# Performance work log

Hardware: AMD Instinct MI355X
Metric: run time of the kernel (lower is better)

The kernel has to match this reference:

```python
import jax, jax.numpy as jnp
import numpy as np
from jax import lax

N, C, H, W = 8, 512, 28, 28
G = 8                     # attention groups
QKP = 32                  # qk_planes = out/groups/2
VP = 64                   # v_planes = branch/groups
BP = 512                  # branch_planes
HW = H * W
EPS = 1e-5                # BatchNorm eps (eval mode, running_mean=0, running_var=1)


def bn(x, gamma, beta, axis=1):
    shape = [1] * x.ndim
    shape[axis] = x.shape[axis]
    g = gamma.reshape(shape)
    b = beta.reshape(shape)
    return x * (g / jnp.sqrt(1.0 + EPS)) + b


def conv2d(x, w, groups=1):
    return lax.conv_general_dilated(
        x, w, (1, 1), 'SAME',
        dimension_numbers=('NCHW', 'OIHW', 'NCHW'),
        feature_group_count=groups)


def setup_inputs() -> dict:
    key = jax.random.key(0)
    ks = jax.random.split(key, 16)
    pe_dim = 2 * QKP + VP  # 128
    inp = {
        'x':        jax.random.normal(ks[0], (N, C, H, W), jnp.float32),
        'qkv_w':    jax.random.normal(ks[1], (BP * 2, C), jnp.float32) * np.sqrt(1.0 / C),
        'g_qkv':    jax.random.normal(ks[2], (BP * 2,), jnp.float32) * 0.1 + 1.0,
        'b_qkv':    jax.random.normal(ks[3], (BP * 2,), jnp.float32) * 0.1,
        'g_sim':    jax.random.normal(ks[4], (G * 3,), jnp.float32) * 0.1 + 1.0,
        'b_sim':    jax.random.normal(ks[5], (G * 3,), jnp.float32) * 0.1,
        'g_out':    jax.random.normal(ks[6], (BP * 2,), jnp.float32) * 0.1 + 1.0,
        'b_out':    jax.random.normal(ks[7], (BP * 2,), jnp.float32) * 0.1,
        'relative': jax.random.normal(ks[8], (pe_dim, 2 * HW - 1), jnp.float32) * np.sqrt(1.0 / VP),
        'xw1':      jax.random.normal(ks[9], (BP, C // G, 3, 3), jnp.float32) * np.sqrt(2.0 / (C // G * 9)),
        'xw2':      jax.random.normal(ks[10], (BP, BP, 1, 1), jnp.float32) * np.sqrt(2.0 / BP),
        'g_x':      jnp.ones((BP,), jnp.float32),
        'b_x':      jnp.zeros((BP,), jnp.float32),
        'rw':       jax.random.normal(ks[11], (BP, BP * 2, 1, 1), jnp.float32) * np.sqrt(2.0 / (BP * 2)),
        'g_r':      jnp.ones((BP,), jnp.float32),
        'b_r':      jnp.zeros((BP,), jnp.float32),
        'pw':       jax.random.normal(ks[12], (BP, BP, 1, 1), jnp.float32) * np.sqrt(2.0 / BP),
        'g_p':      jnp.ones((BP,), jnp.float32),
        'b_p':      jnp.zeros((BP,), jnp.float32),
    }
    return inp


def reference(x, qkv_w, g_qkv, b_qkv, g_sim, b_sim, g_out, b_out, relative,
              xw1, xw2, g_x, b_x, rw, g_r, b_r, pw, g_p, b_p):
    n = x.shape[0]
    # ---- unary branch: grouped 3x3 conv + 1x1 conv + BN ----
    unary = conv2d(x, xw1, groups=G)
    unary = conv2d(unary, xw2)
    unary = bn(unary, g_x, b_x)

    # ---- binary branch (attention over HW tokens) ----
    xf = x.reshape(n, C, HW)
    qkv = jnp.einsum('oc,bci->boi', qkv_w, xf)          # Conv1d k=1
    qkv = bn(qkv, g_qkv, b_qkv)
    qkv = qkv.reshape(n, G, 2 * QKP + VP, HW)
    q = qkv[:, :, :QKP]
    k = qkv[:, :, QKP:2 * QKP]
    v = qkv[:, :, 2 * QKP:]

    # relative position embeddings via index gather: emb[c,i,j] = relative[c, i-j+HW-1]
    idx = jnp.arange(HW)
    rel_idx = idx[:, None] - idx[None, :] + HW - 1      # [HW, HW]
    emb = relative[:, rel_idx]                           # [pe_dim, HW, HW]
    q_emb, k_emb, v_emb = emb[:QKP], emb[QKP:2 * QKP], emb[2 * QKP:]

    qk = jnp.einsum('bgci,bgcj->bgij', q, k)
    qr = jnp.einsum('bgci,cij->bgij', q, q_emb)
    kr = jnp.einsum('bgci,cij->bgij', k, k_emb).swapaxes(2, 3)
    stacked = jnp.concatenate([qk, qr, kr], axis=1)      # [n, 3G, HW, HW]
    stacked = bn(stacked, g_sim, b_sim)
    logits = stacked.reshape(n, 3, G, HW, HW).sum(axis=1)
    sim = jax.nn.softmax(logits, axis=-1)                # softmax over keys j

    sv = jnp.einsum('bgij,bgcj->bgci', sim, v)
    sve = jnp.einsum('bgij,cij->bgci', sim, v_emb)
    stacked_binary = jnp.concatenate([sv, sve], axis=-1).reshape(n, BP * 2, HW)
    stacked_binary = bn(stacked_binary, g_out, b_out)
    binary = stacked_binary.reshape(n, BP, 2, HW).sum(axis=2).reshape(n, BP, H, W)

    # ---- gating / reasoning path ----
    gate_in = jnp.concatenate([unary, binary], axis=1)   # [n, 2*BP, H, W]
    r = jax.nn.relu(gate_in)
    r = jax.nn.relu(bn(conv2d(r, rw), g_r, b_r))
    gate = jax.nn.sigmoid(bn(conv2d(r, pw), g_p, b_p))

    return gate * binary + unary


if __name__ == '__main__':
    out = reference(**setup_inputs())
    print(out.shape, out.dtype)
```

## Files before the change

kernel.cpp:

```cpp
#include <hip/hip_runtime.h>
#include <math.h>


typedef unsigned short u16;
typedef unsigned int u32;
typedef __bf16 bf16x8 __attribute__((ext_vector_type(8)));
typedef float f32x4 __attribute__((ext_vector_type(4)));

#define INVS 0.99999500003749968f
#define MFMA16(a, b, c) __builtin_amdgcn_mfma_f32_16x16x32_bf16(a, b, c, 0, 0, 0)

__device__ inline u16 f2bf(float f) {
  u32 u = __builtin_bit_cast(u32, f);
  return (u16)((u + 0x7fffu + ((u >> 16) & 1u)) >> 16);
}
__device__ inline float bf2f(u16 h) {
  u32 u = ((u32)h) << 16;
  return __builtin_bit_cast(float, u);
}
__device__ inline bf16x8 ld_bf8(const u16* p) {
  int4 v = *reinterpret_cast<const int4*>(p);
  return __builtin_bit_cast(bf16x8, v);
}
__device__ inline bf16x8 pack8(const u16 h[8]) {
  int4 v;
  v.x = (int)((u32)h[0] | ((u32)h[1] << 16));
  v.y = (int)((u32)h[2] | ((u32)h[3] << 16));
  v.z = (int)((u32)h[4] | ((u32)h[5] << 16));
  v.w = (int)((u32)h[6] | ((u32)h[7] << 16));
  return __builtin_bit_cast(bf16x8, v);
}
__device__ inline bf16x8 zero8() {
  int4 z = {0, 0, 0, 0};
  return __builtin_bit_cast(bf16x8, z);
}
__device__ inline float bpermf(float v, int srcl) {
  return __builtin_bit_cast(float,
      __builtin_amdgcn_ds_bpermute(srcl << 2, __builtin_bit_cast(int, v)));
}
__device__ inline int4 relu8(int4 v) {
  u32* w = reinterpret_cast<u32*>(&v);
#pragma unroll
  for (int k = 0; k < 4; ++k) {
    u32 x = w[k];
    u32 s = (x >> 15) & 0x00010001u;
    w[k] = x & ((0x00010001u - s) * 0xFFFFu);
  }
  return v;
}


__device__ void body_prep(
    int idx, const float* __restrict__ qkv_w, const float* __restrict__ xw2,
    const float* __restrict__ rw, const float* __restrict__ pw,
    const float* __restrict__ xw1, const float* __restrict__ rel,
    u16* __restrict__ Wq, u16* __restrict__ W2, u16* __restrict__ Wr,
    u16* __restrict__ Wp, u16* __restrict__ W1t, u16* __restrict__ relq,
    u16* __restrict__ relk, u16* __restrict__ relv) {
  if (idx < 524288) { Wq[idx] = f2bf(qkv_w[idx]); return; }
  idx -= 524288;
  if (idx < 262144) { W2[idx] = f2bf(xw2[idx]); return; }
  idx -= 262144;
  if (idx < 524288) { Wr[idx] = f2bf(rw[idx]); return; }
  idx -= 524288;
  if (idx < 262144) { Wp[idx] = f2bf(pw[idx]); return; }
  idx -= 262144;
  if (idx < 294912) {
    int gk = idx >> 12, rem = idx & 4095, oc = rem >> 6, ic = rem & 63;
    int g = gk / 9, k9 = gk % 9;
    W1t[idx] = f2bf(xw1[(((g * 64 + oc) * 64) + ic) * 9 + k9]);
    return;
  }
  idx -= 294912;
  if (idx < 51200) {
    int t = idx >> 5, c = idx & 31;
    relq[idx] = (t < 1567) ? f2bf(rel[c * 1567 + t]) : (u16)0;
    return;
  }
  idx -= 51200;
  if (idx < 51200) {
    int t = idx >> 5, c = idx & 31;
    relk[idx] = (t < 1567) ? f2bf(rel[(32 + c) * 1567 + t]) : (u16)0;
    return;
  }
  idx -= 51200;
  if (idx < 102400) {
    int c = idx / 1600, t = idx % 1600;
    relv[idx] = (t < 1567) ? f2bf(rel[(64 + c) * 1567 + t]) : (u16)0;
    return;
  }
}

__device__ void body_transpose(int bx, int by, int bz, const float* __restrict__ x,
                               u16* __restrict__ xT, char* smem) {
  const int b = bz, c0 = by * 64, n0 = bx * 32;
  const int tid = threadIdx.x;
  u16(*tl)[36] = reinterpret_cast<u16(*)[36]>(smem);
#pragma unroll
  for (int h = 0; h < 2; ++h) {
    int cl = (tid >> 3) + h * 32;
    int n4 = (tid & 7) * 4;
    float4 v = {0.f, 0.f, 0.f, 0.f};
    if (n0 + n4 + 3 < 784)
      v = *reinterpret_cast<const float4*>(x + ((size_t)b * 512 + c0 + cl) * 784 + n0 + n4);
    u32 lo = (u32)f2bf(v.x) | ((u32)f2bf(v.y) << 16);
    u32 hi = (u32)f2bf(v.z) | ((u32)f2bf(v.w) << 16);
    *reinterpret_cast<int2*>(&tl[cl][n4]) = make_int2((int)lo, (int)hi);
  }
  __syncthreads();
  int nl = tid >> 3, c8 = (tid & 7) * 8;
  if (n0 + nl < 784) {
    u16 h[8];
#pragma unroll
    for (int e = 0; e < 8; ++e) h[e] = tl[c8 + e][nl];
    *reinterpret_cast<int4*>(xT + ((size_t)b * 784 + n0 + nl) * 512 + c0 + c8) =
        __builtin_bit_cast(int4, pack8(h));
  }
}

__device__ void body_qkv(int bx, int by, int bz,
                         const u16* __restrict__ W, const u16* __restrict__ xT,
                         const float* __restrict__ gq, const float* __restrict__ bq,
                         u16* __restrict__ Qs, u16* __restrict__ Ks,
                         u16* __restrict__ Vs, char* smem) {
  const int b = bz, mt = by, n0 = bx * 112;
  const int tid = threadIdx.x, lane = tid & 63, wave = tid >> 6;
  const int lm = lane & 15, lq = lane >> 4;
  u16* Bl = reinterpret_cast<u16*>(smem);
  f32x4 zf = {0.f, 0.f, 0.f, 0.f};
  f32x4 acc[7];
#pragma unroll
  for (int t = 0; t < 7; ++t) acc[t] = zf;
  const u16* Bb = xT + ((size_t)b * 784 + n0) * 512;
  const u16* Ar = W + (size_t)(mt * 64 + wave * 16 + lm) * 512;
  const int row0 = tid >> 2, seg8 = (tid & 3) * 8;
  const u16* src0 = Bb + (size_t)row0 * 512 + seg8;
  const u16* src1 = src0 + (size_t)64 * 512;
  u16* dst0 = &Bl[row0 * 40 + seg8];
  u16* dst1 = &Bl[(row0 + 64) * 40 + seg8];
  int4 p0 = *reinterpret_cast<const int4*>(src0);
  int4 p1;
  if (tid < 192) p1 = *reinterpret_cast<const int4*>(src1);
  bf16x8 afc = ld_bf8(Ar + lq * 8);
  for (int ks = 0; ks < 16; ++ks) {
    *reinterpret_cast<int4*>(dst0) = p0;
    if (tid < 192) *reinterpret_cast<int4*>(dst1) = p1;
    __syncthreads();
    bf16x8 af = afc;
    if (ks < 15) {
      p0 = *reinterpret_cast<const int4*>(src0 + (ks + 1) * 32);
      if (tid < 192) p1 = *reinterpret_cast<const int4*>(src1 + (ks + 1) * 32);
      afc = ld_bf8(Ar + (ks + 1) * 32 + lq * 8);
    }
#pragma unroll
    for (int t = 0; t < 7; ++t) {
      bf16x8 bf8 = ld_bf8(&Bl[(t * 16 + lm) * 40 + lq * 8]);
      acc[t] = MFMA16(af, bf8, acc[t]);
    }
    __syncthreads();
  }
  const int og = mt * 64 + wave * 16 + lq * 4;
  float sc[4], bi[4];
#pragma unroll
  for (int r = 0; r < 4; ++r) { sc[r] = gq[og + r] * INVS; bi[r] = bq[og + r]; }
  const int g = og >> 7, r128 = og & 127;
  const size_t bg = (size_t)b * 8 + g;
#pragma unroll
  for (int t = 0; t < 7; ++t) {
    int j = n0 + t * 16 + lm;
    u16 h[4];
#pragma unroll
    for (int r = 0; r < 4; ++r) h[r] = f2bf(acc[t][r] * sc[r] + bi[r]);
    if (r128 < 64) {
      u16* dst = (r128 < 32) ? Qs : Ks;
      int c = r128 & 31;
      u32 lo = (u32)h[0] | ((u32)h[1] << 16);
      u32 hi = (u32)h[2] | ((u32)h[3] << 16);
      *reinterpret_cast<int2*>(dst + (bg * 784 + j) * 32 + c) = make_int2((int)lo, (int)hi);
    } else {
      int c = r128 - 64;
#pragma unroll
      for (int r = 0; r < 4; ++r) Vs[(bg * 64 + c + r) * 784 + j] = h[r];
    }
  }
}

__device__ void body_conv1(int bx, int by, int bz, const u16* __restrict__ xT,
                           const u16* __restrict__ W1t, u16* __restrict__ umid,
                           char* smem) {
  const int b = bz, g = by, n0 = bx * 112;
  const int tid = threadIdx.x, lane = tid & 63, wave = tid >> 6;
  const int lm = lane & 15, lq = lane >> 4;
  u16* xl = reinterpret_cast<u16*>(smem);
  for (int u = tid; u < 1360; u += 256) {
    int row = u >> 3, seg = u & 7;
    int ng = n0 - 29 + row;
    int4 v = {0, 0, 0, 0};
    if (ng >= 0 && ng < 784)
      v = *reinterpret_cast<const int4*>(xT + ((size_t)b * 784 + ng) * 512 + g * 64 + seg * 8);
    *reinterpret_cast<int4*>(&xl[row * 72 + seg * 8]) = v;
  }
  __syncthreads();
  f32x4 zf = {0.f, 0.f, 0.f, 0.f};
  f32x4 acc[7];
#pragma unroll
  for (int t = 0; t < 7; ++t) acc[t] = zf;
  const u16* Wg = W1t + (size_t)g * 9 * 4096;
#pragma unroll
  for (int k9 = 0; k9 < 9; ++k9) {
    const int dh = k9 / 3 - 1, dw = k9 % 3 - 1;
#pragma unroll
    for (int ks = 0; ks < 2; ++ks) {
      bf16x8 af = ld_bf8(Wg + (k9 * 64 + wave * 16 + lm) * 64 + ks * 32 + lq * 8);
#pragma unroll
      for (int t = 0; t < 7; ++t) {
        int n = n0 + t * 16 + lm;
        int ww = n % 28 + dw;
        bf16x8 bf8;
        if (ww >= 0 && ww < 28)
          bf8 = ld_bf8(&xl[(t * 16 + lm + dh * 28 + dw + 29) * 72 + ks * 32 + lq * 8]);
        else
          bf8 = zero8();
        acc[t] = MFMA16(af, bf8, acc[t]);
      }
    }
  }
  const int oc4 = g * 64 + wave * 16 + lq * 4;
#pragma unroll
  for (int t = 0; t < 7; ++t) {
    int j = n0 + t * 16 + lm;
    u16 h[4];
#pragma unroll
    for (int r = 0; r < 4; ++r) h[r] = f2bf(acc[t][r]);
    u32 lo = (u32)h[0] | ((u32)h[1] << 16);
    u32 hi = (u32)h[2] | ((u32)h[3] << 16);
    *reinterpret_cast<int2*>(umid + ((size_t)b * 784 + j) * 512 + oc4) = make_int2((int)lo, (int)hi);
  }
}

__device__ void body_x2(int bx, int by, int bz,
                        const u16* __restrict__ W, const u16* __restrict__ Bsrc,
                        const float* __restrict__ gv, const float* __restrict__ bv,
                        u16* __restrict__ outB, char* smem) {
  const int b = bz, mt = by, n0 = bx * 112;
  const int tid = threadIdx.x, lane = tid & 63, wave = tid >> 6;
  const int lm = lane & 15, lq = lane >> 4;
  u16* Bl = reinterpret_cast<u16*>(smem);
  f32x4 zf = {0.f, 0.f, 0.f, 0.f};
  f32x4 acc[7];
#pragma unroll
  for (int t = 0; t < 7; ++t) acc[t] = zf;
  const u16* Bb = Bsrc + ((size_t)b * 784 + n0) * 512;
  const u16* Ar = W + (size_t)(mt * 64 + wave * 16 + lm) * 512;
  for (int ks = 0; ks < 16; ++ks) {
    __syncthreads();
    for (int u = tid; u < 448; u += 256) {
      int row = u >> 2, seg = u & 3;
      int4 v = *reinterpret_cast<const int4*>(Bb + (size_t)row * 512 + ks * 32 + seg * 8);
      *reinterpret_cast<int4*>(&Bl[row * 40 + seg * 8]) = v;
    }
    __syncthreads();
    bf16x8 af = ld_bf8(Ar + ks * 32 + lq * 8);
#pragma unroll
    for (int t = 0; t < 7; ++t) {
      bf16x8 bf8 = ld_bf8(&Bl[(t * 16 + lm) * 40 + lq * 8]);
      acc[t] = MFMA16(af, bf8, acc[t]);
    }
  }
  const int og = mt * 64 + wave * 16 + lq * 4;
  float sc[4], bi[4];
#pragma unroll
  for (int r = 0; r < 4; ++r) { sc[r] = gv[og + r] * INVS; bi[r] = bv[og + r]; }
#pragma unroll
  for (int t = 0; t < 7; ++t) {
    int j = n0 + t * 16 + lm;
    u16 h[4];
#pragma unroll
    for (int r = 0; r < 4; ++r) h[r] = f2bf(acc[t][r] * sc[r] + bi[r]);
    u32 lo = (u32)h[0] | ((u32)h[1] << 16);
    u32 hi = (u32)h[2] | ((u32)h[3] << 16);
    *reinterpret_cast<int2*>(outB + ((size_t)b * 784 + j) * 512 + og) = make_int2((int)lo, (int)hi);
  }
}

__device__ void body_attn(int bx, int by, int bz,
                          const u16* __restrict__ Qs, const u16* __restrict__ Ks,
                          const u16* __restrict__ Vs, const u16* __restrict__ relq,
                          const u16* __restrict__ relk, const u16* __restrict__ relv,
                          const float* __restrict__ g_sim, const float* __restrict__ g_out,
                          const float* __restrict__ b_out, u16* __restrict__ binB,
                          char* smem) {
  const int b = bz, g = by, i0 = bx * 16;
  const int tid = threadIdx.x, lane = tid & 63, wave = tid >> 6;
  const int lm = lane & 15, lq = lane >> 4;
  u16* Pl = reinterpret_cast<u16*>(smem);
  float* KRs = reinterpret_cast<float*>(smem + 27936);
  float* WM = reinterpret_cast<float*>(smem + 36640);
  float* rstat = reinterpret_cast<float*>(smem + 36896);
  for (int u = tid; u < 1424; u += 256) {
    int idx = (u < 16) ? u : (16 + ((u - 16) / 88) * 872 + 784 + (u - 16) % 88);
    Pl[idx] = 0;
  }
  const float s0 = g_sim[g] * INVS, s1 = g_sim[8 + g] * INVS, s2 = g_sim[16 + g] * INVS;
  const size_t bg = (size_t)b * 8 + g;
  const u16* Qb = Qs + bg * 784 * 32;
  const u16* Kb = Ks + bg * 784 * 32;
  const u16* Vb = Vs + bg * 64 * 784;
  const bf16x8 aq = ld_bf8(Qb + (i0 + lm) * 32 + lq * 8);
  const f32x4 zf = {0.f, 0.f, 0.f, 0.f};
  float vmax[4] = {-1e30f, -1e30f, -1e30f, -1e30f};
  bf16x8 kfc, bq0c, bq1c, bk0c, bk1c;
  {
    const int j0 = wave * 16;
    const int d0 = 768 + i0 - j0, e0 = 768 + j0 - i0;
    kfc = ld_bf8(Kb + (j0 + lm) * 32 + lq * 8);
    bq0c = ld_bf8(relq + (d0 + lm) * 32 + lq * 8);
    bq1c = ld_bf8(relq + (d0 + 16 + lm) * 32 + lq * 8);
    bk0c = ld_bf8(relk + (e0 + lm) * 32 + lq * 8);
    bk1c = ld_bf8(relk + (e0 + 16 + lm) * 32 + lq * 8);
  }
  int jt = wave;
  for (int rr = 0; rr < 13; ++rr) {
    const int jtn = jt + 4;
    bf16x8 kfn = kfc, bq0n = bq0c, bq1n = bq1c, bk0n = bk0c, bk1n = bk1c;
    if (jtn < 49) {
      const int j0n = jtn * 16;
      const int d0 = 768 + i0 - j0n, e0 = 768 + j0n - i0;
      kfn = ld_bf8(Kb + (j0n + lm) * 32 + lq * 8);
      bq0n = ld_bf8(relq + (d0 + lm) * 32 + lq * 8);
      bq1n = ld_bf8(relq + (d0 + 16 + lm) * 32 + lq * 8);
      bk0n = ld_bf8(relk + (e0 + lm) * 32 + lq * 8);
      bk1n = ld_bf8(relk + (e0 + 16 + lm) * 32 + lq * 8);
    }
    if (jt < 49) {
      const int j0 = jt * 16;
      f32x4 aqk = MFMA16(aq, kfc, zf);
      f32x4 q0 = MFMA16(aq, bq0c, zf);
      f32x4 q1 = MFMA16(aq, bq1c, zf);
      f32x4 k0 = MFMA16(kfc, bk0c, zf);
      f32x4 k1 = MFMA16(kfc, bk1c, zf);
#pragma unroll
      for (int r = 0; r < 4; ++r) {
        int m = lq * 4 + r;
        KRs[(wave * 16 + m) * 34 + lm] = k0[r];
        KRs[(wave * 16 + m) * 34 + 16 + lm] = k1[r];
      }
#pragma unroll
      for (int r = 0; r < 4; ++r) {
        int m = lq * 4 + r, n = lm;
        int c = m - n + 15;
        int srcl = (c & 15) | (lane & 48);
        float t0 = bpermf(q0[r], srcl), t1 = bpermf(q1[r], srcl);
        float qv = (c & 16) ? t1 : t0;
        float kv = KRs[(wave * 16 + n) * 34 + (n - m + 15)];
        float val = aqk[r] * s0 + qv * s1 + kv * s2;
        vmax[r] = fmaxf(vmax[r], val);
        _Float16 hv = (_Float16)val;
        Pl[16 + m * 872 + j0 + n] = __builtin_bit_cast(u16, hv);
      }
    }
    jt = jtn;
    kfc = kfn; bq0c = bq0n; bq1c = bq1n; bk0c = bk0n; bk1c = bk1n;
  }
#pragma unroll
  for (int r = 0; r < 4; ++r) {
#pragma unroll
    for (int d = 1; d < 16; d <<= 1) vmax[r] = fmaxf(vmax[r], __shfl_xor(vmax[r], d, 64));
  }
  if (lm == 0) {
#pragma unroll
    for (int r = 0; r < 4; ++r) WM[wave * 16 + lq * 4 + r] = vmax[r];
  }
  __syncthreads();
  {
    const int row = tid >> 4, sub = tid & 15;
    u16* Pr = &Pl[16 + row * 872];
    float gmax = fmaxf(fmaxf(WM[row], WM[16 + row]), fmaxf(WM[32 + row], WM[48 + row]));
    float sm = 0.f;
    for (int c = sub; c < 98; c += 16) {
      int4 v = *reinterpret_cast<int4*>(&Pr[c * 8]);
      u16* hh = reinterpret_cast<u16*>(&v);
      u16 oo[8];
#pragma unroll
      for (int e = 0; e < 8; ++e) {
        float ev = __expf((float)__builtin_bit_cast(_Float16, hh[e]) - gmax);
        sm += ev;
        oo[e] = f2bf(ev);
      }
      *reinterpret_cast<int4*>(&Pr[c * 8]) = __builtin_bit_cast(int4, pack8(oo));
    }
#pragma unroll
    for (int d = 1; d < 16; d <<= 1) sm += __shfl_xor(sm, d, 64);
    if (sub == 0) rstat[row] = 1.0f / sm;
  }
  __syncthreads();
  f32x4 accV = zf, accE = zf;
  const int coff = wave * 16;
  const u16* Vr = Vb + (size_t)(coff + lm) * 784;
  const u16* Rr = relv + (size_t)(coff + lm) * 1600 + i0;
  const u16* Prow = &Pl[16 + lm * 872];
  for (int ks = 0; ks < 25; ++ks) {
    bf16x8 ap = ld_bf8(Prow + ks * 32 + lq * 8);
    bf16x8 bv = ld_bf8(Vr + ks * 32 + lq * 8);
    accV = MFMA16(ap, bv, accV);
    const int base = 783 + lm - ks * 32 - lq * 8;
    u16 h[8];
#pragma unroll
    for (int e = 0; e < 8; ++e) h[e] = Prow[base - e];
    bf16x8 ash = pack8(h);
    bf16x8 br = ld_bf8(Rr + ks * 32 + lq * 8);
    accE = MFMA16(ash, br, accE);
  }
  const int c = coff + lm;
  const int oi = g * 128 + 2 * c;
  const float so0 = g_out[oi] * INVS, bo0 = b_out[oi];
  const float so1 = g_out[oi + 1] * INVS, bo1 = b_out[oi + 1];
#pragma unroll
  for (int r = 0; r < 4; ++r) {
    int row = lq * 4 + r;
    float rl = rstat[row];
    float val = accV[r] * rl * so0 + bo0 + accE[r] * rl * so1 + bo1;
    binB[((size_t)b * 784 + i0 + row) * 512 + g * 64 + c] = f2bf(val);
  }
}


__global__ __launch_bounds__(256) void k_pt(
    const float* __restrict__ x, u16* __restrict__ xT,
    const float* __restrict__ qkv_w, const float* __restrict__ xw2,
    const float* __restrict__ rw, const float* __restrict__ pw,
    const float* __restrict__ xw1, const float* __restrict__ rel,
    u16* __restrict__ Wq, u16* __restrict__ W2, u16* __restrict__ Wr,
    u16* __restrict__ Wp, u16* __restrict__ W1t, u16* __restrict__ relq,
    u16* __restrict__ relk, u16* __restrict__ relv) {
  __shared__ __align__(16) char smem[4608];
  const int bid = blockIdx.x;
  if (bid < 1600) {
    body_transpose(bid % 25, (bid / 25) % 8, bid / 200, x, xT, smem);
  } else {
    body_prep((bid - 1600) * 256 + threadIdx.x, qkv_w, xw2, rw, pw, xw1, rel,
              Wq, W2, Wr, Wp, W1t, relq, relk, relv);
  }
}

__global__ __launch_bounds__(256) void k_qc(
    const u16* __restrict__ Wq, const u16* __restrict__ xT,
    const float* __restrict__ gq, const float* __restrict__ bq,
    u16* __restrict__ Qs, u16* __restrict__ Ks, u16* __restrict__ Vs,
    const u16* __restrict__ W1t, u16* __restrict__ umid) {
  __shared__ __align__(16) char smem[24480];
  const int bid = blockIdx.x;
  if (bid < 448) {
    body_conv1(bid % 7, (bid / 7) % 8, bid / 56, xT, W1t, umid, smem);
  } else {
    const int q = bid - 448;
    body_qkv(q % 7, (q / 7) % 16, q / 112, Wq, xT, gq, bq, Qs, Ks, Vs, smem);
  }
}

__global__ __launch_bounds__(256, 8) void k_ax(
    const u16* __restrict__ W2, const u16* __restrict__ umid,
    const float* __restrict__ g_x, const float* __restrict__ b_x,
    u16* __restrict__ unB,
    const u16* __restrict__ Qs, const u16* __restrict__ Ks, const u16* __restrict__ Vs,
    const u16* __restrict__ relq, const u16* __restrict__ relk,
    const u16* __restrict__ relv, const float* __restrict__ g_sim,
    const float* __restrict__ g_out, const float* __restrict__ b_out,
    u16* __restrict__ binB) {
  __shared__ __align__(16) char smem[36960];
  const int bid = blockIdx.x;
  if (bid < 448) {
    body_x2(bid % 7, (bid / 7) % 8, bid / 56, W2, umid, g_x, b_x, unB, smem);
  } else {
    const int a = bid - 448;
    body_attn(a % 49, (a / 49) % 8, a / 392, Qs, Ks, Vs, relq, relk, relv,
              g_sim, g_out, b_out, binB, smem);
  }
}

__global__ __launch_bounds__(256) void k_gemm_rw(
    const u16* __restrict__ W, const u16* __restrict__ unB, const u16* __restrict__ binB,
    const float* __restrict__ gv, const float* __restrict__ bv, u16* __restrict__ rT) {
  const int b = blockIdx.z, mt = blockIdx.y, n0 = blockIdx.x * 112;
  const int tid = threadIdx.x, lane = tid & 63, wave = tid >> 6;
  const int lm = lane & 15, lq = lane >> 4;
  __shared__ __align__(16) u16 Bl[112 * 40];
  f32x4 zf = {0.f, 0.f, 0.f, 0.f};
  f32x4 acc[7];
#pragma unroll
  for (int t = 0; t < 7; ++t) acc[t] = zf;
  const u16* Ar = W + (size_t)(mt * 64 + wave * 16 + lm) * 1024;
  const int row0 = tid >> 2, seg8 = (tid & 3) * 8;
  const size_t off0 = ((size_t)b * 784 + n0 + row0) * 512 + seg8;
  const size_t off1 = off0 + (size_t)64 * 512;
  u16* dst0 = &Bl[row0 * 40 + seg8];
  u16* dst1 = &Bl[(row0 + 64) * 40 + seg8];
  int4 p0 = *reinterpret_cast<const int4*>(unB + off0);
  int4 p1;
  if (tid < 192) p1 = *reinterpret_cast<const int4*>(unB + off1);
  bf16x8 afc = ld_bf8(Ar + lq * 8);
  for (int ks = 0; ks < 32; ++ks) {
    *reinterpret_cast<int4*>(dst0) = relu8(p0);
    if (tid < 192) *reinterpret_cast<int4*>(dst1) = relu8(p1);
    __syncthreads();
    bf16x8 af = afc;
    if (ks < 31) {
      const int ksn = ks + 1;
      const u16* sb = (ksn < 16) ? unB : binB;
      const int k0 = (ksn & 15) * 32;
      p0 = *reinterpret_cast<const int4*>(sb + off0 + k0);
      if (tid < 192) p1 = *reinterpret_cast<const int4*>(sb + off1 + k0);
      afc = ld_bf8(Ar + ksn * 32 + lq * 8);
    }
#pragma unroll
    for (int t = 0; t < 7; ++t) {
      bf16x8 bf8 = ld_bf8(&Bl[(t * 16 + lm) * 40 + lq * 8]);
      acc[t] = MFMA16(af, bf8, acc[t]);
    }
    __syncthreads();
  }
  const int og = mt * 64 + wave * 16 + lq * 4;
  float sc[4], bi[4];
#pragma unroll
  for (int r = 0; r < 4; ++r) { sc[r] = gv[og + r] * INVS; bi[r] = bv[og + r]; }
#pragma unroll
  for (int t = 0; t < 7; ++t) {
    int j = n0 + t * 16 + lm;
    u16 h[4];
#pragma unroll
    for (int r = 0; r < 4; ++r) h[r] = f2bf(fmaxf(acc[t][r] * sc[r] + bi[r], 0.f));
    u32 lo = (u32)h[0] | ((u32)h[1] << 16);
    u32 hi = (u32)h[2] | ((u32)h[3] << 16);
    *reinterpret_cast<int2*>(rT + ((size_t)b * 784 + j) * 512 + og) = make_int2((int)lo, (int)hi);
  }
}

__global__ __launch_bounds__(256) void k_gemm_pw(
    const u16* __restrict__ W, const u16* __restrict__ rT,
    const float* __restrict__ gv, const float* __restrict__ bv,
    const u16* __restrict__ binB, const u16* __restrict__ unB,
    float* __restrict__ out) {
  const int b = blockIdx.z, mt = blockIdx.y, n0 = blockIdx.x * 112;
  const int tid = threadIdx.x, lane = tid & 63, wave = tid >> 6;
  const int lm = lane & 15, lq = lane >> 4;
  __shared__ __align__(16) u16 Bl[112 * 40];
  f32x4 zf = {0.f, 0.f, 0.f, 0.f};
  f32x4 acc[7];
#pragma unroll
  for (int t = 0; t < 7; ++t) acc[t] = zf;
  const u16* Bb = rT + ((size_t)b * 784 + n0) * 512;
  const u16* Ar = W + (size_t)(mt * 64 + wave * 16 + lm) * 512;
  const int row0 = tid >> 2, seg8 = (tid & 3) * 8;
  const u16* src0 = Bb + (size_t)row0 * 512 + seg8;
  const u16* src1 = src0 + (size_t)64 * 512;
  u16* dst0 = &Bl[row0 * 40 + seg8];
  u16* dst1 = &Bl[(row0 + 64) * 40 + seg8];
  int4 p0 = *reinterpret_cast<const int4*>(src0);
  int4 p1;
  if (tid < 192) p1 = *reinterpret_cast<const int4*>(src1);
  bf16x8 afc = ld_bf8(Ar + lq * 8);
  for (int ks = 0; ks < 16; ++ks) {
    *reinterpret_cast<int4*>(dst0) = p0;
    if (tid < 192) *reinterpret_cast<int4*>(dst1) = p1;
    __syncthreads();
    bf16x8 af = afc;
    if (ks < 15) {
      p0 = *reinterpret_cast<const int4*>(src0 + (ks + 1) * 32);
      if (tid < 192) p1 = *reinterpret_cast<const int4*>(src1 + (ks + 1) * 32);
      afc = ld_bf8(Ar + (ks + 1) * 32 + lq * 8);
    }
#pragma unroll
    for (int t = 0; t < 7; ++t) {
      bf16x8 bf8 = ld_bf8(&Bl[(t * 16 + lm) * 40 + lq * 8]);
      acc[t] = MFMA16(af, bf8, acc[t]);
    }
    __syncthreads();
  }
  const int og = mt * 64 + wave * 16 + lq * 4;
  float sc[4], bi[4];
#pragma unroll
  for (int r = 0; r < 4; ++r) { sc[r] = gv[og + r] * INVS; bi[r] = bv[og + r]; }
#pragma unroll
  for (int t = 0; t < 7; ++t) {
    int j = n0 + t * 16 + lm;
    size_t ofs = ((size_t)b * 784 + j) * 512 + og;
    int2 b2 = *reinterpret_cast<const int2*>(binB + ofs);
    int2 u2 = *reinterpret_cast<const int2*>(unB + ofs);
    const u16* bh = reinterpret_cast<const u16*>(&b2);
    const u16* uh = reinterpret_cast<const u16*>(&u2);
#pragma unroll
    for (int r = 0; r < 4; ++r) {
      float gt = 1.f / (1.f + __expf(-(acc[t][r] * sc[r] + bi[r])));
      out[((size_t)b * 512 + og + r) * 784 + j] = gt * bf2f(bh[r]) + bf2f(uh[r]);
    }
  }
}

extern "C" void kernel_launch(void* const* d_in, const int* in_sizes, int n_in,
                              void* d_out, int out_size, void* d_ws, size_t ws_size,
                              hipStream_t stream) {
  const float* x = (const float*)d_in[0];
  const float* qkv_w = (const float*)d_in[1];
  const float* g_qkv = (const float*)d_in[2];
  const float* b_qkv = (const float*)d_in[3];
  const float* g_sim = (const float*)d_in[4];
  const float* g_out = (const float*)d_in[6];
  const float* b_out = (const float*)d_in[7];
  const float* relative = (const float*)d_in[8];
  const float* xw1 = (const float*)d_in[9];
  const float* xw2 = (const float*)d_in[10];
  const float* g_x = (const float*)d_in[11];
  const float* b_x = (const float*)d_in[12];
  const float* rw = (const float*)d_in[13];
  const float* g_r = (const float*)d_in[14];
  const float* b_r = (const float*)d_in[15];
  const float* pw = (const float*)d_in[16];
  const float* g_p = (const float*)d_in[17];
  const float* b_p = (const float*)d_in[18];

  char* p = (char*)d_ws;
  auto take = [&](size_t n) { char* q = p; p += (n + 255) & ~(size_t)255; return q; };
  u16* xT = (u16*)take((size_t)8 * 784 * 512 * 2);
  u16* Wq = (u16*)take((size_t)1024 * 512 * 2);
  u16* W2 = (u16*)take((size_t)512 * 512 * 2);
  u16* Wr = (u16*)take((size_t)512 * 1024 * 2);
  u16* Wp = (u16*)take((size_t)512 * 512 * 2);
  u16* W1t = (u16*)take((size_t)294912 * 2);
  u16* relq = (u16*)take((size_t)51200 * 2);
  u16* relk = (u16*)take((size_t)51200 * 2);
  u16* relv = (u16*)take((size_t)102400 * 2);
  u16* Qs = (u16*)take((size_t)8 * 8 * 784 * 32 * 2);
  u16* Ks = (u16*)take((size_t)8 * 8 * 784 * 32 * 2);
  u16* Vs = (u16*)take(((size_t)8 * 8 * 64 * 784 + 64) * 2);
  u16* umid = (u16*)take((size_t)8 * 784 * 512 * 2);
  u16* unB = (u16*)take((size_t)8 * 784 * 512 * 2);
  u16* binB = (u16*)take((size_t)8 * 784 * 512 * 2);
  u16* rT = (u16*)take((size_t)8 * 784 * 512 * 2);

  k_pt<<<dim3(9696), dim3(256), 0, stream>>>(x, xT, qkv_w, xw2, rw, pw, xw1, relative,
                                             Wq, W2, Wr, Wp, W1t, relq, relk, relv);
  k_qc<<<dim3(1344), dim3(256), 0, stream>>>(Wq, xT, g_qkv, b_qkv, Qs, Ks, Vs, W1t, umid);
  k_ax<<<dim3(3584), dim3(256), 0, stream>>>(W2, umid, g_x, b_x, unB, Qs, Ks, Vs,
                                             relq, relk, relv, g_sim, g_out, b_out, binB);
  k_gemm_rw<<<dim3(7, 8, 8), dim3(256), 0, stream>>>(Wr, unB, binB, g_r, b_r, rT);
  k_gemm_pw<<<dim3(7, 8, 8), dim3(256), 0, stream>>>(Wp, rT, g_p, b_p, binB, unB,
                                                     (float*)d_out);
}
```

Baseline: 296.0 us.

## Split fused x2/attention kernel and shrink attention shared memory

Splits the combined k_ax launch into two separate kernels, k_x2 and k_attn, so each gets its own shared-memory footprint and launch bounds. Attention now uses a smaller padded P row stride and stores the key-relative tile as bf16 instead of fp32, which cuts LDS per block so more blocks can be resident. The x2 GEMM gains register prefetch of the next B and A tiles to overlap global loads with MFMA. The split adds a launch and removes the overlap of the two workloads within a single grid. Storing key-relative logits in bf16 also lowers their precision.

```diff
diff --git a/kernel.cpp b/kernel.cpp
--- a/kernel.cpp
+++ b/kernel.cpp
@@ -238,34 +238,79 @@
   }
 }
 
-__device__ void body_x2(int bx, int by, int bz,
-                        const u16* __restrict__ W, const u16* __restrict__ Bsrc,
-                        const float* __restrict__ gv, const float* __restrict__ bv,
-                        u16* __restrict__ outB, char* smem) {
-  const int b = bz, mt = by, n0 = bx * 112;
+
+__global__ __launch_bounds__(256) void k_pt(
+    const float* __restrict__ x, u16* __restrict__ xT,
+    const float* __restrict__ qkv_w, const float* __restrict__ xw2,
+    const float* __restrict__ rw, const float* __restrict__ pw,
+    const float* __restrict__ xw1, const float* __restrict__ rel,
+    u16* __restrict__ Wq, u16* __restrict__ W2, u16* __restrict__ Wr,
+    u16* __restrict__ Wp, u16* __restrict__ W1t, u16* __restrict__ relq,
+    u16* __restrict__ relk, u16* __restrict__ relv) {
+  __shared__ __align__(16) char smem[4608];
+  const int bid = blockIdx.x;
+  if (bid < 1600) {
+    body_transpose(bid % 25, (bid / 25) % 8, bid / 200, x, xT, smem);
+  } else {
+    body_prep((bid - 1600) * 256 + threadIdx.x, qkv_w, xw2, rw, pw, xw1, rel,
+              Wq, W2, Wr, Wp, W1t, relq, relk, relv);
+  }
+}
+
+__global__ __launch_bounds__(256) void k_qc(
+    const u16* __restrict__ Wq, const u16* __restrict__ xT,
+    const float* __restrict__ gq, const float* __restrict__ bq,
+    u16* __restrict__ Qs, u16* __restrict__ Ks, u16* __restrict__ Vs,
+    const u16* __restrict__ W1t, u16* __restrict__ umid) {
+  __shared__ __align__(16) char smem[24480];
+  const int bid = blockIdx.x;
+  if (bid < 448) {
+    body_conv1(bid % 7, (bid / 7) % 8, bid / 56, xT, W1t, umid, smem);
+  } else {
+    const int q = bid - 448;
+    body_qkv(q % 7, (q / 7) % 16, q / 112, Wq, xT, gq, bq, Qs, Ks, Vs, smem);
+  }
+}
+
+__global__ __launch_bounds__(256) void k_x2(
+    const u16* __restrict__ W, const u16* __restrict__ Bsrc,
+    const float* __restrict__ gv, const float* __restrict__ bv,
+    u16* __restrict__ outB) {
+  const int b = blockIdx.z, mt = blockIdx.y, n0 = blockIdx.x * 112;
   const int tid = threadIdx.x, lane = tid & 63, wave = tid >> 6;
   const int lm = lane & 15, lq = lane >> 4;
-  u16* Bl = reinterpret_cast<u16*>(smem);
+  __shared__ __align__(16) u16 Bl[112 * 40];
   f32x4 zf = {0.f, 0.f, 0.f, 0.f};
   f32x4 acc[7];
 #pragma unroll
   for (int t = 0; t < 7; ++t) acc[t] = zf;
   const u16* Bb = Bsrc + ((size_t)b * 784 + n0) * 512;
   const u16* Ar = W + (size_t)(mt * 64 + wave * 16 + lm) * 512;
+  const int row0 = tid >> 2, seg8 = (tid & 3) * 8;
+  const u16* src0 = Bb + (size_t)row0 * 512 + seg8;
+  const u16* src1 = src0 + (size_t)64 * 512;
+  u16* dst0 = &Bl[row0 * 40 + seg8];
+  u16* dst1 = &Bl[(row0 + 64) * 40 + seg8];
+  int4 p0 = *reinterpret_cast<const int4*>(src0);
+  int4 p1;
+  if (tid < 192) p1 = *reinterpret_cast<const int4*>(src1);
+  bf16x8 afc = ld_bf8(Ar + lq * 8);
   for (int ks = 0; ks < 16; ++ks) {
-    __syncthreads();
-    for (int u = tid; u < 448; u += 256) {
-      int row = u >> 2, seg = u & 3;
-      int4 v = *reinterpret_cast<const int4*>(Bb + (size_t)row * 512 + ks * 32 + seg * 8);
-      *reinterpret_cast<int4*>(&Bl[row * 40 + seg * 8]) = v;
-    }
-    __syncthreads();
-    bf16x8 af = ld_bf8(Ar + ks * 32 + lq * 8);
+    *reinterpret_cast<int4*>(dst0) = p0;
+    if (tid < 192) *reinterpret_cast<int4*>(dst1) = p1;
+    __syncthreads();
+    bf16x8 af = afc;
+    if (ks < 15) {
+      p0 = *reinterpret_cast<const int4*>(src0 + (ks + 1) * 32);
+      if (tid < 192) p1 = *reinterpret_cast<const int4*>(src1 + (ks + 1) * 32);
+      afc = ld_bf8(Ar + (ks + 1) * 32 + lq * 8);
+    }
 #pragma unroll
     for (int t = 0; t < 7; ++t) {
       bf16x8 bf8 = ld_bf8(&Bl[(t * 16 + lm) * 40 + lq * 8]);
       acc[t] = MFMA16(af, bf8, acc[t]);
     }
+    __syncthreads();
   }
   const int og = mt * 64 + wave * 16 + lq * 4;
   float sc[4], bi[4];
@@ -283,22 +328,20 @@
   }
 }
 
-__device__ void body_attn(int bx, int by, int bz,
-                          const u16* __restrict__ Qs, const u16* __restrict__ Ks,
-                          const u16* __restrict__ Vs, const u16* __restrict__ relq,
-                          const u16* __restrict__ relk, const u16* __restrict__ relv,
-                          const float* __restrict__ g_sim, const float* __restrict__ g_out,
-                          const float* __restrict__ b_out, u16* __restrict__ binB,
-                          char* smem) {
-  const int b = bz, g = by, i0 = bx * 16;
+__global__ __launch_bounds__(256) void k_attn(
+    const u16* __restrict__ Qs, const u16* __restrict__ Ks, const u16* __restrict__ Vs,
+    const u16* __restrict__ relq, const u16* __restrict__ relk, const u16* __restrict__ relv,
+    const float* __restrict__ g_sim, const float* __restrict__ g_out,
+    const float* __restrict__ b_out, u16* __restrict__ binB) {
+  const int b = blockIdx.z, g = blockIdx.y, i0 = blockIdx.x * 16;
   const int tid = threadIdx.x, lane = tid & 63, wave = tid >> 6;
   const int lm = lane & 15, lq = lane >> 4;
-  u16* Pl = reinterpret_cast<u16*>(smem);
-  float* KRs = reinterpret_cast<float*>(smem + 27936);
-  float* WM = reinterpret_cast<float*>(smem + 36640);
-  float* rstat = reinterpret_cast<float*>(smem + 36896);
-  for (int u = tid; u < 1424; u += 256) {
-    int idx = (u < 16) ? u : (16 + ((u - 16) / 88) * 872 + 784 + (u - 16) % 88);
+  __shared__ __align__(16) u16 Pl[16 + 16 * 824];
+  __shared__ __align__(4) u16 KRsH[4 * 16 * 34];
+  __shared__ float WM[64];
+  __shared__ float rstat[16];
+  for (int u = tid; u < 656; u += 256) {
+    int idx = (u < 16) ? u : (16 + ((u - 16) / 40) * 824 + 784 + (u - 16) % 40);
     Pl[idx] = 0;
   }
   const float s0 = g_sim[g] * INVS, s1 = g_sim[8 + g] * INVS, s2 = g_sim[16 + g] * INVS;
@@ -342,8 +385,8 @@
 #pragma unroll
       for (int r = 0; r < 4; ++r) {
         int m = lq * 4 + r;
-        KRs[(wave * 16 + m) * 34 + lm] = k0[r];
-        KRs[(wave * 16 + m) * 34 + 16 + lm] = k1[r];
+        KRsH[(wave * 16 + m) * 34 + lm] = f2bf(k0[r]);
+        KRsH[(wave * 16 + m) * 34 + 16 + lm] = f2bf(k1[r]);
       }
 #pragma unroll
       for (int r = 0; r < 4; ++r) {
@@ -352,11 +395,11 @@
         int srcl = (c & 15) | (lane & 48);
         float t0 = bpermf(q0[r], srcl), t1 = bpermf(q1[r], srcl);
         float qv = (c & 16) ? t1 : t0;
-        float kv = KRs[(wave * 16 + n) * 34 + (n - m + 15)];
+        float kv = bf2f(KRsH[(wave * 16 + n) * 34 + (n - m + 15)]);
         float val = aqk[r] * s0 + qv * s1 + kv * s2;
         vmax[r] = fmaxf(vmax[r], val);
         _Float16 hv = (_Float16)val;
-        Pl[16 + m * 872 + j0 + n] = __builtin_bit_cast(u16, hv);
+        Pl[16 + m * 824 + j0 + n] = __builtin_bit_cast(u16, hv);
       }
     }
     jt = jtn;
@@ -374,7 +417,7 @@
   __syncthreads();
   {
     const int row = tid >> 4, sub = tid & 15;
-    u16* Pr = &Pl[16 + row * 872];
+    u16* Pr = &Pl[16 + row * 824];
     float gmax = fmaxf(fmaxf(WM[row], WM[16 + row]), fmaxf(WM[32 + row], WM[48 + row]));
     float sm = 0.f;
     for (int c = sub; c < 98; c += 16) {
@@ -398,7 +441,7 @@
   const int coff = wave * 16;
   const u16* Vr = Vb + (size_t)(coff + lm) * 784;
   const u16* Rr = relv + (size_t)(coff + lm) * 1600 + i0;
-  const u16* Prow = &Pl[16 + lm * 872];
+  const u16* Prow = &Pl[16 + lm * 824];
   for (int ks = 0; ks < 25; ++ks) {
     bf16x8 ap = ld_bf8(Prow + ks * 32 + lq * 8);
     bf16x8 bv = ld_bf8(Vr + ks * 32 + lq * 8);
@@ -421,60 +464,6 @@
     float rl = rstat[row];
     float val = accV[r] * rl * so0 + bo0 + accE[r] * rl * so1 + bo1;
     binB[((size_t)b * 784 + i0 + row) * 512 + g * 64 + c] = f2bf(val);
-  }
-}
-
-
-__global__ __launch_bounds__(256) void k_pt(
-    const float* __restrict__ x, u16* __restrict__ xT,
-    const float* __restrict__ qkv_w, const float* __restrict__ xw2,
-    const float* __restrict__ rw, const float* __restrict__ pw,
-    const float* __restrict__ xw1, const float* __restrict__ rel,
-    u16* __restrict__ Wq, u16* __restrict__ W2, u16* __restrict__ Wr,
-    u16* __restrict__ Wp, u16* __restrict__ W1t, u16* __restrict__ relq,
-    u16* __restrict__ relk, u16* __restrict__ relv) {
-  __shared__ __align__(16) char smem[4608];
-  const int bid = blockIdx.x;
-  if (bid < 1600) {
-    body_transpose(bid % 25, (bid / 25) % 8, bid / 200, x, xT, smem);
-  } else {
-    body_prep((bid - 1600) * 256 + threadIdx.x, qkv_w, xw2, rw, pw, xw1, rel,
-              Wq, W2, Wr, Wp, W1t, relq, relk, relv);
-  }
-}
-
-__global__ __launch_bounds__(256) void k_qc(
-    const u16* __restrict__ Wq, const u16* __restrict__ xT,
-    const float* __restrict__ gq, const float* __restrict__ bq,
-    u16* __restrict__ Qs, u16* __restrict__ Ks, u16* __restrict__ Vs,
-    const u16* __restrict__ W1t, u16* __restrict__ umid) {
-  __shared__ __align__(16) char smem[24480];
-  const int bid = blockIdx.x;
-  if (bid < 448) {
-    body_conv1(bid % 7, (bid / 7) % 8, bid / 56, xT, W1t, umid, smem);
-  } else {
-    const int q = bid - 448;
-    body_qkv(q % 7, (q / 7) % 16, q / 112, Wq, xT, gq, bq, Qs, Ks, Vs, smem);
-  }
-}
-
-__global__ __launch_bounds__(256, 8) void k_ax(
-    const u16* __restrict__ W2, const u16* __restrict__ umid,
-    const float* __restrict__ g_x, const float* __restrict__ b_x,
-    u16* __restrict__ unB,
-    const u16* __restrict__ Qs, const u16* __restrict__ Ks, const u16* __restrict__ Vs,
-    const u16* __restrict__ relq, const u16* __restrict__ relk,
-    const u16* __restrict__ relv, const float* __restrict__ g_sim,
-    const float* __restrict__ g_out, const float* __restrict__ b_out,
-    u16* __restrict__ binB) {
-  __shared__ __align__(16) char smem[36960];
-  const int bid = blockIdx.x;
-  if (bid < 448) {
-    body_x2(bid % 7, (bid / 7) % 8, bid / 56, W2, umid, g_x, b_x, unB, smem);
-  } else {
-    const int a = bid - 448;
-    body_attn(a % 49, (a / 49) % 8, a / 392, Qs, Ks, Vs, relq, relk, relv,
-              g_sim, g_out, b_out, binB, smem);
   }
 }
 
@@ -640,8 +629,9 @@
   k_pt<<<dim3(9696), dim3(256), 0, stream>>>(x, xT, qkv_w, xw2, rw, pw, xw1, relative,
                                              Wq, W2, Wr, Wp, W1t, relq, relk, relv);
   k_qc<<<dim3(1344), dim3(256), 0, stream>>>(Wq, xT, g_qkv, b_qkv, Qs, Ks, Vs, W1t, umid);
-  k_ax<<<dim3(3584), dim3(256), 0, stream>>>(W2, umid, g_x, b_x, unB, Qs, Ks, Vs,
-                                             relq, relk, relv, g_sim, g_out, b_out, binB);
+  k_x2<<<dim3(7, 8, 8), dim3(256), 0, stream>>>(W2, umid, g_x, b_x, unB);
+  k_attn<<<dim3(49, 8, 8), dim3(256), 0, stream>>>(Qs, Ks, Vs, relq, relk, relv,
+                                                   g_sim, g_out, b_out, binB);
   k_gemm_rw<<<dim3(7, 8, 8), dim3(256), 0, stream>>>(Wr, unB, binB, g_r, b_r, rT);
   k_gemm_pw<<<dim3(7, 8, 8), dim3(256), 0, stream>>>(Wp, rT, g_p, b_p, binB, unB,
                                                      (float*)d_out);
```

Result: no change. 298.5 us (+0.8%).
